# Kernel optimization log

Measured on AMD Instinct MI355X. Metric: run time of the kernel, lower is better.

Reference implementation:

```python
import jax, jax.numpy as jnp
import numpy as np

NO_EDGE_OFFSET_T_NORM = 1.0    # added to the no_edge branch for the T-norm (min) operator
NO_EDGE_OFFSET_T_CONORM = -1.0  # added to the no_edge branch for the T-conorm (max) operator

B, IN_F, OUT_F = 2048, 256, 256
N_EDGE_TYPES, N_OPS = 2, 2


def setup_inputs() -> dict:
    key = jax.random.key(0)
    k1, k2, k3 = jax.random.split(key, 3)
    x = jax.random.uniform(k1, (B, IN_F), dtype=jnp.float32)
    prob_edge_weights = jax.random.normal(k2, (OUT_F, IN_F, N_EDGE_TYPES), dtype=jnp.float32)
    prob_node_weights = jax.random.normal(k3, (OUT_F, N_OPS), dtype=jnp.float32)
    return {"x": x, "prob_edge_weights": prob_edge_weights, "prob_node_weights": prob_node_weights}


def reference(x, prob_edge_weights, prob_node_weights):
    # train_mode = train_both: softmax over edge types and over operators
    edge_prob = jax.nn.softmax(prob_edge_weights, axis=-1)  # [O, I, E]
    node_prob = jax.nn.softmax(prob_node_weights, axis=-1)  # [O, U]

    p_edge = edge_prob[:, :, 0]     # prob of real edge (identity transform), [O, I]
    p_noedge = edge_prob[:, :, 1]   # prob of no_edge (zeros + operator-specific offset), [O, I]

    # expected edge value per (batch, out, in); the no_edge branch contributes
    # offset * p_noedge since its edge_value is zeros(x) + offset.
    base = x[:, None, :] * p_edge   # [B, O, I]

    # operator 0: T-norm (min over in_features), no_edge offset = +1
    ev_min = jnp.min(base + NO_EDGE_OFFSET_T_NORM * p_noedge, axis=-1)    # [B, O]
    # operator 1: T-conorm (max over in_features), no_edge offset = -1
    ev_max = jnp.max(base + NO_EDGE_OFFSET_T_CONORM * p_noedge, axis=-1)  # [B, O]

    # expectation over operators
    return ev_min * node_prob[:, 0] + ev_max * node_prob[:, 1]  # [B, O]
```

## Files before the change

### kernel.cpp

```cpp
#include <hip/hip_runtime.h>
#include <math.h>

#define BT 32
#define OT 32
#define IT 128
#define NTHREADS 256
#define IN_F 256
#define OUT_F 256

__global__ __launch_bounds__(NTHREADS, 2)
void den_kernel(const float* __restrict__ x,
                const float* __restrict__ pew,
                const float* __restrict__ pnw,
                float* __restrict__ out, int B)
{
    __shared__ __align__(16) float x_lds[IT][BT + 1];
    __shared__ __align__(16) float pe_lds[IT][OT + 4];

    const int tid = threadIdx.x;
    const int tb  = tid & 31;
    const int to  = tid >> 5;
    const int b0  = blockIdx.x * BT;
    const int o0  = blockIdx.y * OT;

    const int srow = tid >> 3;
    const int sc   = tid & 7;

    float accmin0 = INFINITY,  accmin1 = INFINITY,  accmin2 = INFINITY,  accmin3 = INFINITY;
    float accmax0 = -INFINITY, accmax1 = -INFINITY, accmax2 = -INFINITY, accmax3 = -INFINITY;

    for (int it = 0; it < IN_F; it += IT) {
        if (it) __syncthreads();

        const float4* xg = reinterpret_cast<const float4*>(x + (size_t)(b0 + srow) * IN_F + it);
        #pragma unroll
        for (int k = 0; k < 4; ++k) {
            float4 g = xg[sc + 8 * k];
            int il = (sc + 8 * k) * 4;
            x_lds[il + 0][srow] = g.x - 1.0f;
            x_lds[il + 1][srow] = g.y - 1.0f;
            x_lds[il + 2][srow] = g.z - 1.0f;
            x_lds[il + 3][srow] = g.w - 1.0f;
        }

        const float4* wg = reinterpret_cast<const float4*>(pew + ((size_t)(o0 + srow) * IN_F + it) * 2);
        #pragma unroll
        for (int k = 0; k < 8; ++k) {
            float4 w = wg[sc + 8 * k];
            int il = (sc + 8 * k) * 2;
            float e0 = __expf(w.y - w.x);
            float e1 = __expf(w.w - w.z);
            pe_lds[il + 0][srow] = __builtin_amdgcn_rcpf(1.0f + e0);
            pe_lds[il + 1][srow] = __builtin_amdgcn_rcpf(1.0f + e1);
        }
        __syncthreads();

        #pragma unroll 4
        for (int i = 0; i < IT; i += 2) {
            float xm0 = x_lds[i + 0][tb];
            float xm1 = x_lds[i + 1][tb];
            float4 p0 = *reinterpret_cast<const float4*>(&pe_lds[i + 0][to * 4]);
            float4 p1 = *reinterpret_cast<const float4*>(&pe_lds[i + 1][to * 4]);

            { float t0 = xm0 * p0.x, t1 = xm1 * p1.x;
              float u0 = __builtin_fmaf(2.0f, p0.x, t0), u1 = __builtin_fmaf(2.0f, p1.x, t1);
              accmin0 = fminf(fminf(accmin0, t0), t1);
              accmax0 = fmaxf(fmaxf(accmax0, u0), u1); }
            { float t0 = xm0 * p0.y, t1 = xm1 * p1.y;
              float u0 = __builtin_fmaf(2.0f, p0.y, t0), u1 = __builtin_fmaf(2.0f, p1.y, t1);
              accmin1 = fminf(fminf(accmin1, t0), t1);
              accmax1 = fmaxf(fmaxf(accmax1, u0), u1); }
            { float t0 = xm0 * p0.z, t1 = xm1 * p1.z;
              float u0 = __builtin_fmaf(2.0f, p0.z, t0), u1 = __builtin_fmaf(2.0f, p1.z, t1);
              accmin2 = fminf(fminf(accmin2, t0), t1);
              accmax2 = fmaxf(fmaxf(accmax2, u0), u1); }
            { float t0 = xm0 * p0.w, t1 = xm1 * p1.w;
              float u0 = __builtin_fmaf(2.0f, p0.w, t0), u1 = __builtin_fmaf(2.0f, p1.w, t1);
              accmin3 = fminf(fminf(accmin3, t0), t1);
              accmax3 = fmaxf(fmaxf(accmax3, u0), u1); }
        }
    }

    const int o = o0 + to * 4;
    float4 nw0 = *reinterpret_cast<const float4*>(pnw + 2 * (size_t)o);
    float4 nw1 = *reinterpret_cast<const float4*>(pnw + 2 * (size_t)o + 4);
    float4 r;
    { float n0 = __builtin_amdgcn_rcpf(1.0f + __expf(nw0.y - nw0.x));
      r.x = (accmin0 + 1.0f) * n0 + (accmax0 - 1.0f) * (1.0f - n0); }
    { float n0 = __builtin_amdgcn_rcpf(1.0f + __expf(nw0.w - nw0.z));
      r.y = (accmin1 + 1.0f) * n0 + (accmax1 - 1.0f) * (1.0f - n0); }
    { float n0 = __builtin_amdgcn_rcpf(1.0f + __expf(nw1.y - nw1.x));
      r.z = (accmin2 + 1.0f) * n0 + (accmax2 - 1.0f) * (1.0f - n0); }
    { float n0 = __builtin_amdgcn_rcpf(1.0f + __expf(nw1.w - nw1.z));
      r.w = (accmin3 + 1.0f) * n0 + (accmax3 - 1.0f) * (1.0f - n0); }
    *reinterpret_cast<float4*>(out + (size_t)(b0 + tb) * OUT_F + o) = r;
}

extern "C" void kernel_launch(void* const* d_in, const int* in_sizes, int n_in,
                              void* d_out, int out_size, void* d_ws, size_t ws_size,
                              hipStream_t stream) {
    const float* x   = (const float*)d_in[0];
    const float* pew = (const float*)d_in[1];
    const float* pnw = (const float*)d_in[2];
    float* out = (float*)d_out;
    int B = in_sizes[0] / IN_F;
    dim3 grid(B / BT, OUT_F / OT);
    den_kernel<<<grid, NTHREADS, 0, stream>>>(x, pew, pnw, out, B);
}
```

Measured before the change: 71.86 us.

## Restructure tiling: full-row swizzled edge-prob tile in LDS, x read from global

Each block now handles 64 output features and 16 batch rows. It precomputes the whole 64x256 edge-probability tile into LDS once, using an XOR swizzle to avoid bank conflicts. Each lane owns one output feature and loops over the inputs, reading x as wave-uniform float4 loads straight from global memory instead of staging it through LDS. This removes the x staging, the inner-loop LDS traffic for x and the repeated barriers. In exchange it uses 64KB of LDS per block, which may limit occupancy, and stores outputs as scalars rather than float4.

```diff
diff --git a/kernel.cpp b/kernel.cpp
--- a/kernel.cpp
+++ b/kernel.cpp
@@ -1,109 +1,96 @@
 #include <hip/hip_runtime.h>
 #include <math.h>
 
-#define BT 32
-#define OT 32
-#define IT 128
-#define NTHREADS 256
-#define IN_F 256
+#define IN_F  256
 #define OUT_F 256
+#define OTILE 64
+#define BTILE 16
+#define NTH   256
 
-__global__ __launch_bounds__(NTHREADS, 2)
+__global__ __launch_bounds__(NTH, 2)
 void den_kernel(const float* __restrict__ x,
                 const float* __restrict__ pew,
                 const float* __restrict__ pnw,
-                float* __restrict__ out, int B)
+                float* __restrict__ out)
 {
-    __shared__ __align__(16) float x_lds[IT][BT + 1];
-    __shared__ __align__(16) float pe_lds[IT][OT + 4];
+    __shared__ float pe_lds[OTILE * IN_F];
 
     const int tid = threadIdx.x;
-    const int tb  = tid & 31;
-    const int to  = tid >> 5;
-    const int b0  = blockIdx.x * BT;
-    const int o0  = blockIdx.y * OT;
+    const int b0  = blockIdx.x * BTILE;
+    const int o0  = blockIdx.y * OTILE;
 
-    const int srow = tid >> 3;
-    const int sc   = tid & 7;
+    {
+        const int r16 = tid >> 4;
+        const int c   = tid & 15;
+        for (int rg = 0; rg < 4; ++rg) {
+            const int o  = rg * 16 + r16;
+            const int xm = (o & 7) << 4;
+            const float4* wp = reinterpret_cast<const float4*>(pew + (size_t)(o0 + o) * (IN_F * 2));
+            char* rowp = reinterpret_cast<char*>(&pe_lds[o * IN_F]);
+            #pragma unroll
+            for (int k = 0; k < 8; ++k) {
+                float4 w = wp[k * 16 + c];
+                float pe0 = __builtin_amdgcn_rcpf(1.0f + __expf(w.y - w.x));
+                float pe1 = __builtin_amdgcn_rcpf(1.0f + __expf(w.w - w.z));
+                const int byteoff = (8 * (k * 16 + c)) ^ xm;
+                *reinterpret_cast<float2*>(rowp + byteoff) = make_float2(pe0, pe1);
+            }
+        }
+    }
+    __syncthreads();
 
-    float accmin0 = INFINITY,  accmin1 = INFINITY,  accmin2 = INFINITY,  accmin3 = INFINITY;
-    float accmax0 = -INFINITY, accmax1 = -INFINITY, accmax2 = -INFINITY, accmax3 = -INFINITY;
+    const int lane = tid & 63;
+    const int wid  = __builtin_amdgcn_readfirstlane(tid >> 6);
+    const int bb0  = b0 + wid * 4;
+    const char* rowp = reinterpret_cast<const char*>(&pe_lds[lane * IN_F]);
+    const int xm = (lane & 7) << 4;
 
-    for (int it = 0; it < IN_F; it += IT) {
-        if (it) __syncthreads();
+    float mn[4], mx[4];
+    #pragma unroll
+    for (int j = 0; j < 4; ++j) { mn[j] = INFINITY; mx[j] = -INFINITY; }
 
-        const float4* xg = reinterpret_cast<const float4*>(x + (size_t)(b0 + srow) * IN_F + it);
+    const float* xr0 = x + (size_t)bb0 * IN_F;
+
+    #pragma unroll 4
+    for (int c = 0; c < 64; ++c) {
+        float4 pv = *reinterpret_cast<const float4*>(rowp + ((16 * c) ^ xm));
         #pragma unroll
-        for (int k = 0; k < 4; ++k) {
-            float4 g = xg[sc + 8 * k];
-            int il = (sc + 8 * k) * 4;
-            x_lds[il + 0][srow] = g.x - 1.0f;
-            x_lds[il + 1][srow] = g.y - 1.0f;
-            x_lds[il + 2][srow] = g.z - 1.0f;
-            x_lds[il + 3][srow] = g.w - 1.0f;
-        }
-
-        const float4* wg = reinterpret_cast<const float4*>(pew + ((size_t)(o0 + srow) * IN_F + it) * 2);
-        #pragma unroll
-        for (int k = 0; k < 8; ++k) {
-            float4 w = wg[sc + 8 * k];
-            int il = (sc + 8 * k) * 2;
-            float e0 = __expf(w.y - w.x);
-            float e1 = __expf(w.w - w.z);
-            pe_lds[il + 0][srow] = __builtin_amdgcn_rcpf(1.0f + e0);
-            pe_lds[il + 1][srow] = __builtin_amdgcn_rcpf(1.0f + e1);
-        }
-        __syncthreads();
-
-        #pragma unroll 4
-        for (int i = 0; i < IT; i += 2) {
-            float xm0 = x_lds[i + 0][tb];
-            float xm1 = x_lds[i + 1][tb];
-            float4 p0 = *reinterpret_cast<const float4*>(&pe_lds[i + 0][to * 4]);
-            float4 p1 = *reinterpret_cast<const float4*>(&pe_lds[i + 1][to * 4]);
-
-            { float t0 = xm0 * p0.x, t1 = xm1 * p1.x;
-              float u0 = __builtin_fmaf(2.0f, p0.x, t0), u1 = __builtin_fmaf(2.0f, p1.x, t1);
-              accmin0 = fminf(fminf(accmin0, t0), t1);
-              accmax0 = fmaxf(fmaxf(accmax0, u0), u1); }
-            { float t0 = xm0 * p0.y, t1 = xm1 * p1.y;
-              float u0 = __builtin_fmaf(2.0f, p0.y, t0), u1 = __builtin_fmaf(2.0f, p1.y, t1);
-              accmin1 = fminf(fminf(accmin1, t0), t1);
-              accmax1 = fmaxf(fmaxf(accmax1, u0), u1); }
-            { float t0 = xm0 * p0.z, t1 = xm1 * p1.z;
-              float u0 = __builtin_fmaf(2.0f, p0.z, t0), u1 = __builtin_fmaf(2.0f, p1.z, t1);
-              accmin2 = fminf(fminf(accmin2, t0), t1);
-              accmax2 = fmaxf(fmaxf(accmax2, u0), u1); }
-            { float t0 = xm0 * p0.w, t1 = xm1 * p1.w;
-              float u0 = __builtin_fmaf(2.0f, p0.w, t0), u1 = __builtin_fmaf(2.0f, p1.w, t1);
-              accmin3 = fminf(fminf(accmin3, t0), t1);
-              accmax3 = fmaxf(fmaxf(accmax3, u0), u1); }
+        for (int j = 0; j < 4; ++j) {
+            float4 xv = *reinterpret_cast<const float4*>(xr0 + j * IN_F + 4 * c);
+            float t0 = __builtin_fmaf(xv.x, pv.x, -pv.x);
+            float t1 = __builtin_fmaf(xv.y, pv.y, -pv.y);
+            float t2 = __builtin_fmaf(xv.z, pv.z, -pv.z);
+            float t3 = __builtin_fmaf(xv.w, pv.w, -pv.w);
+            float u0 = __builtin_fmaf(2.0f, pv.x, t0);
+            float u1 = __builtin_fmaf(2.0f, pv.y, t1);
+            float u2 = __builtin_fmaf(2.0f, pv.z, t2);
+            float u3 = __builtin_fmaf(2.0f, pv.w, t3);
+            mn[j] = fminf(fminf(mn[j], t0), t1);
+            mn[j] = fminf(fminf(mn[j], t2), t3);
+            mx[j] = fmaxf(fmaxf(mx[j], u0), u1);
+            mx[j] = fmaxf(fmaxf(mx[j], u2), u3);
         }
     }
 
-    const int o = o0 + to * 4;
-    float4 nw0 = *reinterpret_cast<const float4*>(pnw + 2 * (size_t)o);
-    float4 nw1 = *reinterpret_cast<const float4*>(pnw + 2 * (size_t)o + 4);
-    float4 r;
-    { float n0 = __builtin_amdgcn_rcpf(1.0f + __expf(nw0.y - nw0.x));
-      r.x = (accmin0 + 1.0f) * n0 + (accmax0 - 1.0f) * (1.0f - n0); }
-    { float n0 = __builtin_amdgcn_rcpf(1.0f + __expf(nw0.w - nw0.z));
-      r.y = (accmin1 + 1.0f) * n0 + (accmax1 - 1.0f) * (1.0f - n0); }
-    { float n0 = __builtin_amdgcn_rcpf(1.0f + __expf(nw1.y - nw1.x));
-      r.z = (accmin2 + 1.0f) * n0 + (accmax2 - 1.0f) * (1.0f - n0); }
-    { float n0 = __builtin_amdgcn_rcpf(1.0f + __expf(nw1.w - nw1.z));
-      r.w = (accmin3 + 1.0f) * n0 + (accmax3 - 1.0f) * (1.0f - n0); }
-    *reinterpret_cast<float4*>(out + (size_t)(b0 + tb) * OUT_F + o) = r;
+    const int o = o0 + lane;
+    float2 nw = *reinterpret_cast<const float2*>(pnw + 2 * (size_t)o);
+    float n0 = __builtin_amdgcn_rcpf(1.0f + __expf(nw.y - nw.x));
+    float n1 = 1.0f - n0;
+    #pragma unroll
+    for (int j = 0; j < 4; ++j) {
+        out[(size_t)(bb0 + j) * OUT_F + o] = (mn[j] + 1.0f) * n0 + (mx[j] - 1.0f) * n1;
+    }
 }
 
 extern "C" void kernel_launch(void* const* d_in, const int* in_sizes, int n_in,
                               void* d_out, int out_size, void* d_ws, size_t ws_size,
                               hipStream_t stream) {
+    (void)d_ws; (void)ws_size; (void)n_in; (void)out_size;
     const float* x   = (const float*)d_in[0];
     const float* pew = (const float*)d_in[1];
     const float* pnw = (const float*)d_in[2];
     float* out = (float*)d_out;
-    int B = in_sizes[0] / IN_F;
-    dim3 grid(B / BT, OUT_F / OT);
-    den_kernel<<<grid, NTHREADS, 0, stream>>>(x, pew, pnw, out, B);
+    const int B = in_sizes[0] / IN_F;
+    dim3 grid(B / BTILE, OUT_F / OTILE);
+    den_kernel<<<grid, NTH, 0, stream>>>(x, pew, pnw, out);
 }
```

After: 73.13 us. No clear change (+1.8%).
